# Kernel optimization log

Hardware: AMD Instinct MI355X
Metric: run time of the kernel (lower is better)

## Reference

```python
import jax, jax.numpy as jnp
import numpy as np

B, S, HID, NH, KCLIP = 2, 1500, 1024, 16, 64
HD = HID // NH  # 64


def setup_inputs() -> dict:
    key = jax.random.key(0)
    ks = jax.random.split(key, 16)
    std = 0.02
    inp = {
        "query": jax.random.normal(ks[0], (B, S, HID), jnp.float32),
        "key": jax.random.normal(ks[1], (B, S, HID), jnp.float32),
        "value": jax.random.normal(ks[2], (B, S, HID), jnp.float32),
        # per-head projection weights, stacked over heads: [NH, HID, HD]
        "Wq": jax.random.normal(ks[3], (NH, HID, HD), jnp.float32) * std,
        "bq": jax.random.normal(ks[4], (NH, HD), jnp.float32) * std,
        "Wk": jax.random.normal(ks[5], (NH, HID, HD), jnp.float32) * std,
        "bk": jax.random.normal(ks[6], (NH, HD), jnp.float32) * std,
        "Wv": jax.random.normal(ks[7], (NH, HID, HD), jnp.float32) * std,
        "bv": jax.random.normal(ks[8], (NH, HD), jnp.float32) * std,
        # Shaw relative-position embedding tables: [2k+1, HD]
        "pe_k": jax.random.normal(ks[9], (2 * KCLIP + 1, HD), jnp.float32) * std,
        "pe_v": jax.random.normal(ks[10], (2 * KCLIP + 1, HD), jnp.float32) * std,
        # output projection (torch Linear stored as x @ W + b here)
        "W_fc": jax.random.normal(ks[11], (HID, HID), jnp.float32) * std,
        "b_fc": jax.random.normal(ks[12], (HID,), jnp.float32) * std,
    }
    return inp


def _rel_bias(pe, length, k_clip):
    idx = jnp.arange(length)
    dist = jnp.clip(idx[None, :] - idx[:, None], -k_clip, k_clip) + k_clip
    return pe[dist]  # [S, S, HD]


def reference(query, key, value, Wq, bq, Wk, bk, Wv, bv, pe_k, pe_v, W_fc, b_fc):
    head_dim = Wq.shape[-1]
    seq = query.shape[1]
    k_clip = (pe_k.shape[0] - 1) // 2

    kb = _rel_bias(pe_k, seq, k_clip)  # [S, S, HD]
    vb = _rel_bias(pe_v, seq, k_clip)  # [S, S, HD]

    # batched per-head projections: [B, NH, S, HD]
    Q = jnp.einsum('bsh,nhd->bnsd', query, Wq) + bq[None, :, None, :]
    K = jnp.einsum('bsh,nhd->bnsd', key, Wk) + bk[None, :, None, :]
    V = jnp.einsum('bsh,nhd->bnsd', value, Wv) + bv[None, :, None, :]

    # content term + Shaw relative-key bias term
    scores = jnp.einsum('bnqd,bnkd->bnqk', Q, K) \
           + jnp.einsum('bnqd,qkd->bnqk', Q, kb)
    scores = scores / jnp.sqrt(jnp.asarray(head_dim, scores.dtype))

    w = jax.nn.softmax(scores, axis=-1)  # [B, NH, S, S]

    out = jnp.einsum('bnqk,bnkd->bnqd', w, V) \
        + jnp.einsum('bnqk,qkd->bnqd', w, vb)

    # concat heads (head order matches ModuleList concatenation)
    hidden = out.transpose(0, 2, 1, 3).reshape(query.shape[0], seq, -1)
    return hidden @ W_fc + b_fc
```

## Files before the change

### kernel.cpp

```cpp
#include <hip/hip_runtime.h>
#include <math.h>

#define B_     2
#define S_     1500
#define HID_   1024
#define NH_    16
#define HD_    64
#define M_     (B_*S_)
#define SP_    1536

typedef short bf16x8 __attribute__((ext_vector_type(8)));
typedef short bf16x4 __attribute__((ext_vector_type(4)));
typedef float f32x4  __attribute__((ext_vector_type(4)));

__device__ __forceinline__ float b2f(short s) {
    unsigned u = ((unsigned)(unsigned short)s) << 16;
    return __uint_as_float(u);
}
__device__ __forceinline__ short f2b(float f) {
    unsigned u = __float_as_uint(f);
    unsigned r = (u + 0x7FFFu + ((u >> 16) & 1u)) >> 16;
    return (short)r;
}
__device__ __forceinline__ void gload16(const short* src, short* lds) {
    __builtin_amdgcn_global_load_lds(
        (const __attribute__((address_space(1))) void*)src,
        (__attribute__((address_space(3))) void*)lds, 16, 0, 0);
}

__global__ __launch_bounds__(256) void cvt_act3(
    const float* __restrict__ q, const float* __restrict__ k,
    const float* __restrict__ v, short* __restrict__ oq,
    short* __restrict__ ok, short* __restrict__ ov)
{
    const float* src = blockIdx.y == 0 ? q : blockIdx.y == 1 ? k : v;
    short* dst       = blockIdx.y == 0 ? oq : blockIdx.y == 1 ? ok : ov;
    int i = blockIdx.x * 256 + threadIdx.x;
    const float4* p = (const float4*)(src + (size_t)i * 8);
    float4 a = p[0], b = p[1];
    bf16x8 o;
    o[0]=f2b(a.x); o[1]=f2b(a.y); o[2]=f2b(a.z); o[3]=f2b(a.w);
    o[4]=f2b(b.x); o[5]=f2b(b.y); o[6]=f2b(b.z); o[7]=f2b(b.w);
    *(bf16x8*)(dst + (size_t)i * 8) = o;
}

__global__ __launch_bounds__(256) void prep_w(
    const float* __restrict__ Wq, const float* __restrict__ Wk,
    const float* __restrict__ Wv, const float* __restrict__ Wfc,
    const float* __restrict__ pe_k, const float* __restrict__ pe_v,
    short* __restrict__ Wqt, short* __restrict__ Wkt, short* __restrict__ Wvt,
    short* __restrict__ Wfh, short* __restrict__ Wfl,
    short* __restrict__ pe_kb, short* __restrict__ pe_vt)
{
    int z = blockIdx.x, tid = threadIdx.x;
    if (z == 1024) {
        for (int s = tid; s < 144 * 64; s += 256) {
            int j = s >> 6, d = s & 63;
            pe_kb[s] = (j < 129) ? f2b(pe_k[j * 64 + d]) : (short)0;
        }
        for (int s = tid; s < 64 * 160; s += 256) {
            int d = s / 160, j = s - d * 160;
            pe_vt[s] = (j < 129) ? f2b(pe_v[j * 64 + d]) : (short)0;
        }
        return;
    }
    __shared__ float T[64][65];
    const float* src; short* dhi; short* dlo = nullptr;
    int C, c0, r0; float scale = 1.f;
    if (z < 768) {
        int widx = z >> 8, rem = z & 255;
        int h = rem >> 4, rt = rem & 15;
        src = (widx == 0 ? Wq : widx == 1 ? Wk : Wv) + (size_t)h * 1024 * 64;
        dhi = (widx == 0 ? Wqt : widx == 1 ? Wkt : Wvt) + (size_t)h * 64 * 1024;
        scale = (widx == 0) ? 0.125f : 1.0f;
        C = 64; c0 = 0; r0 = rt * 64;
    } else {
        int idx = z - 768;
        src = Wfc; dhi = Wfh; dlo = Wfl;
        C = 1024; c0 = (idx >> 4) * 64; r0 = (idx & 15) * 64;
    }
#pragma unroll
    for (int i = 0; i < 4; ++i) {
        int slot = tid + i * 256;
        int r = slot >> 4, cg = (slot & 15) * 4;
        float4 v = *(const float4*)(src + (size_t)(r0 + r) * C + c0 + cg);
        T[r][cg+0] = v.x*scale; T[r][cg+1] = v.y*scale;
        T[r][cg+2] = v.z*scale; T[r][cg+3] = v.w*scale;
    }
    __syncthreads();
#pragma unroll
    for (int i = 0; i < 16; ++i) {
        int slot = tid + i * 256;
        int c = slot >> 6, r = slot & 63;
        float v = T[r][c];
        short hi = f2b(v);
        size_t o = (size_t)(c0 + c) * 1024 + r0 + r;
        dhi[o] = hi;
        if (dlo) dlo[o] = f2b(v - b2f(hi));
    }
}

__device__ __forceinline__ void gemm_core(
    const short* __restrict__ Ahi, const short* __restrict__ Alo,
    const short* __restrict__ Bhi, const short* __restrict__ Blo,
    int kIters, int m0, int n0, short* As, short* Bs, f32x4 (&acc)[4][4])
{
    const int tid = threadIdx.x, w = tid >> 6, lane = tid & 63;
    const int l15 = lane & 15, lr4 = lane >> 4;
    const int wr = w >> 1, wc = w & 1;

    for (int it = 0; it < kIters; ++it) {
        int kt = it * 64;
        int seg = kt >> 10, kk0 = kt & 1023;
        const short* Aseg = (seg == 1) ? Alo : Ahi;
        const short* Bseg = (seg == 2) ? Blo : Bhi;
        __syncthreads();
#pragma unroll
        for (int c = 0; c < 4; ++c) {
            int slot = (w * 4 + c) * 64 + lane;
            int r = slot >> 3, cb = slot & 7;
            int sm = m0 + r; sm = sm < M_ ? sm : M_ - 1;
            gload16(Aseg + (size_t)sm * 1024 + kk0 + ((cb ^ (r & 7)) * 8),
                    As + (size_t)(w * 4 + c) * 512);
            gload16(Bseg + (size_t)(n0 + r) * 1024 + kk0 + ((cb ^ (r & 7)) * 8),
                    Bs + (size_t)(w * 4 + c) * 512);
        }
        __syncthreads();
#pragma unroll
        for (int kh = 0; kh < 2; ++kh) {
            bf16x8 aF[4], bF[4];
#pragma unroll
            for (int mi = 0; mi < 4; ++mi) {
                int r = wr * 64 + mi * 16 + l15;
                aF[mi] = *(const bf16x8*)(As + r * 64 + (((kh*4+lr4) ^ (r & 7)) * 8));
            }
#pragma unroll
            for (int ni = 0; ni < 4; ++ni) {
                int r = wc * 64 + ni * 16 + l15;
                bF[ni] = *(const bf16x8*)(Bs + r * 64 + (((kh*4+lr4) ^ (r & 7)) * 8));
            }
#pragma unroll
            for (int mi = 0; mi < 4; ++mi)
#pragma unroll
                for (int ni = 0; ni < 4; ++ni)
                    acc[mi][ni] = __builtin_amdgcn_mfma_f32_16x16x32_bf16(
                        aF[mi], bF[ni], acc[mi][ni], 0, 0, 0);
        }
    }
}

__global__ __launch_bounds__(256) void gemm_qkv(
    const short* __restrict__ qb, const short* __restrict__ kb,
    const short* __restrict__ vb, const short* __restrict__ Wqt,
    const short* __restrict__ Wkt, const short* __restrict__ Wvt,
    const float* __restrict__ bq, const float* __restrict__ bk,
    const float* __restrict__ bv,
    short* __restrict__ Qp, short* __restrict__ Kp, short* __restrict__ Vp)
{
    __shared__ short As[128 * 64];
    __shared__ short Bs[128 * 64];
    const int z = blockIdx.z;
    const short* A  = z == 0 ? qb : z == 1 ? kb : vb;
    const short* Bw = z == 0 ? Wqt : z == 1 ? Wkt : Wvt;
    const float* bias = z == 0 ? bq : z == 1 ? bk : bv;
    const float bscale = z == 0 ? 0.125f : 1.0f;
    short* out = z == 0 ? Qp : z == 1 ? Kp : Vp;
    const int m0 = blockIdx.x * 128, n0 = blockIdx.y * 128;

    f32x4 zf = {0.f,0.f,0.f,0.f};
    f32x4 acc[4][4];
#pragma unroll
    for (int i = 0; i < 4; ++i)
#pragma unroll
        for (int j = 0; j < 4; ++j) acc[i][j] = zf;

    gemm_core(A, A, Bw, Bw, 16, m0, n0, As, Bs, acc);

    const int tid = threadIdx.x, w = tid >> 6, lane = tid & 63;
    const int l15 = lane & 15, lr4 = lane >> 4;
    const int wr = w >> 1, wc = w & 1;
#pragma unroll
    for (int mi = 0; mi < 4; ++mi)
#pragma unroll
        for (int rr = 0; rr < 4; ++rr) {
            int m = m0 + wr * 64 + mi * 16 + lr4 * 4 + rr;
            if (m >= M_) continue;
            int b = m / S_, s = m - b * S_;
#pragma unroll
            for (int ni = 0; ni < 4; ++ni) {
                int n = n0 + wc * 64 + ni * 16 + l15;
                float v = acc[mi][ni][rr] + bias[n] * bscale;
                int h = n >> 6, d = n & 63;
                out[(((size_t)(b * NH_ + h)) * S_ + s) * HD_ + d] = f2b(v);
            }
        }
}

__global__ __launch_bounds__(256) void gemm_fc(
    const short* __restrict__ Ahi, const short* __restrict__ Alo,
    const short* __restrict__ Bhi, const short* __restrict__ Blo,
    const float* __restrict__ bias, float* __restrict__ out)
{
    __shared__ short As[128 * 64];
    __shared__ short Bs[128 * 64];
    const int m0 = blockIdx.x * 128, n0 = blockIdx.y * 128;
    f32x4 zf = {0.f,0.f,0.f,0.f};
    f32x4 acc[4][4];
#pragma unroll
    for (int i = 0; i < 4; ++i)
#pragma unroll
        for (int j = 0; j < 4; ++j) acc[i][j] = zf;

    gemm_core(Ahi, Alo, Bhi, Blo, 48, m0, n0, As, Bs, acc);

    const int tid = threadIdx.x, w = tid >> 6, lane = tid & 63;
    const int l15 = lane & 15, lr4 = lane >> 4;
    const int wr = w >> 1, wc = w & 1;
#pragma unroll
    for (int mi = 0; mi < 4; ++mi)
#pragma unroll
        for (int rr = 0; rr < 4; ++rr) {
            int m = m0 + wr * 64 + mi * 16 + lr4 * 4 + rr;
            if (m >= M_) continue;
#pragma unroll
            for (int ni = 0; ni < 4; ++ni) {
                int n = n0 + wc * 64 + ni * 16 + l15;
                out[(size_t)m * 1024 + n] = acc[mi][ni][rr] + bias[n];
            }
        }
}

__global__ __launch_bounds__(256) void vtrans(
    const short* __restrict__ Vp, short* __restrict__ Vtg)
{
    __shared__ short T[64][72];
    const int bh = blockIdx.y, s0 = blockIdx.x * 64, tid = threadIdx.x;
    const size_t kv = (size_t)bh * S_ * 64;
#pragma unroll
    for (int i = 0; i < 2; ++i) {
        int slot = tid + i * 256;
        int r = slot >> 3, cb = slot & 7;
        int ss = s0 + r; ss = ss < S_ ? ss : S_ - 1;
        bf16x8 v = *(const bf16x8*)(Vp + kv + (size_t)ss * 64 + cb * 8);
        *(bf16x8*)(&T[r][cb * 8]) = v;
    }
    __syncthreads();
#pragma unroll
    for (int i = 0; i < 2; ++i) {
        int slot = tid + i * 256;
        int d = slot >> 3, cg = slot & 7;
        bf16x8 v;
#pragma unroll
        for (int j = 0; j < 8; ++j) v[j] = T[cg * 8 + j][d];
        *(bf16x8*)(Vtg + ((size_t)bh * 64 + d) * SP_ + s0 + cg * 8) = v;
    }
}

__global__ __launch_bounds__(256) void attn_mfma(
    const short* __restrict__ Qb, const short* __restrict__ Kb,
    const short* __restrict__ Vtg, const short* __restrict__ pe_kb,
    const short* __restrict__ pe_vt,
    short* __restrict__ hid_hi, short* __restrict__ hid_lo)
{
    __shared__ short Kc[64 * 64];
    __shared__ short Vt[64 * 64];
    __shared__ short qpe[64 * 144];
    __shared__ short wsm[64 * 160];
    __shared__ short Pw[4][16 * 64];

    const int tid = threadIdx.x, w = tid >> 6, lane = tid & 63;
    const int l15 = lane & 15, lr4 = lane >> 4;
    const int bh = blockIdx.y, q0 = blockIdx.x * 64;
    const int qw = q0 + w * 16;
    const int myq = qw + l15;
    const int myrow = w * 16 + l15;
    const size_t kv  = (size_t)bh * S_ * HD_;
    const size_t vtb = (size_t)bh * 64 * SP_;
    const int swz = (l15 & 7) << 1;

    {
        short ini = f2b(-1e30f);
        bf16x8 iv;
#pragma unroll
        for (int i = 0; i < 8; ++i) iv[i] = ini;
        for (int s = tid; s < 64 * 160 / 8; s += 256)
            *(bf16x8*)(wsm + (size_t)s * 8) = iv;
    }
#pragma unroll
    for (int c = 0; c < 2; ++c) {
        int slot = (w * 2 + c) * 64 + lane;
        int r = slot >> 3, cb = slot & 7;
        int sq = q0 + r; sq = sq < S_ ? sq : S_ - 1;
        gload16(Qb + kv + (size_t)sq * 64 + ((cb ^ (r & 7)) * 8),
                Kc + (size_t)(w * 2 + c) * 512);
    }
    __syncthreads();

    bf16x8 qA[2];
    {
        int r = myrow;
        qA[0] = *(const bf16x8*)(Kc + r * 64 + ((lr4 ^ (r & 7)) * 8));
        qA[1] = *(const bf16x8*)(Kc + r * 64 + (((4 + lr4) ^ (r & 7)) * 8));
    }

    f32x4 zf = {0.f,0.f,0.f,0.f};
#pragma unroll
    for (int jt = 0; jt < 9; ++jt) {
        f32x4 a = zf;
#pragma unroll
        for (int kh = 0; kh < 2; ++kh) {
            bf16x8 pf = *(const bf16x8*)(pe_kb + (size_t)(jt * 16 + l15) * 64 + kh * 32 + lr4 * 8);
            a = __builtin_amdgcn_mfma_f32_16x16x32_bf16(pf, qA[kh], a, 0, 0, 0);
        }
        bf16x4 pk;
#pragma unroll
        for (int rr = 0; rr < 4; ++rr) pk[rr] = f2b(a[rr]);
        *(bf16x4*)(qpe + (size_t)myrow * 144 + jt * 16 + lr4 * 4) = pk;
    }
    __syncthreads();

    const float qpe0   = b2f(qpe[myrow * 144 + 0]);
    const float qpe128 = b2f(qpe[myrow * 144 + 128]);

    float m = -1e30f, s0s = 0.f, s1s = 0.f;
    f32x4 o[4];
#pragma unroll
    for (int t = 0; t < 4; ++t) o[t] = zf;

    for (int c = 0; c < 24; ++c) {
        const int kc = c * 64;
        __syncthreads();
#pragma unroll
        for (int cc = 0; cc < 2; ++cc) {
            int slot = (w * 2 + cc) * 64 + lane;
            int r = slot >> 3, cb = slot & 7;
            int sk = kc + r; sk = sk < S_ ? sk : S_ - 1;
            gload16(Kb + kv + (size_t)sk * 64 + ((cb ^ (r & 7)) * 8),
                    Kc + (size_t)(w * 2 + cc) * 512);
            gload16(Vtg + vtb + (size_t)r * SP_ + kc + ((cb ^ (r & 7)) * 8),
                    Vt + (size_t)(w * 2 + cc) * 512);
        }
        __syncthreads();

        f32x4 sa[4];
#pragma unroll
        for (int t = 0; t < 4; ++t) {
            sa[t] = zf;
#pragma unroll
            for (int kh = 0; kh < 2; ++kh) {
                int r = t * 16 + l15;
                bf16x8 kB = *(const bf16x8*)(Kc + r * 64 + (((kh*4+lr4) ^ (r & 7)) * 8));
                sa[t] = __builtin_amdgcn_mfma_f32_16x16x32_bf16(kB, qA[kh], sa[t], 0, 0, 0);
            }
        }

        const bool all_lo = (kc + 63 - qw) <= -64;
        const bool all_hi = (kc - (qw + 15)) >= 64;
        const bool mixed  = !(all_lo || all_hi);
        const float ubias = all_lo ? qpe0 : qpe128;

        float lg[4][4];
        float rm = -1e30f;
#pragma unroll
        for (int t = 0; t < 4; ++t)
#pragma unroll
            for (int rr = 0; rr < 4; ++rr) {
                int k = kc + t * 16 + lr4 * 4 + rr;
                int rel = k - myq;
                float v;
                if (mixed) {
                    int jc = rel < -64 ? 0 : (rel > 64 ? 128 : rel + 64);
                    v = sa[t][rr] + b2f(qpe[myrow * 144 + jc]);
                } else {
                    v = sa[t][rr] + ubias;
                }
                if (k >= S_) v = -1e30f;
                lg[t][rr] = v;
                rm = fmaxf(rm, v);
                if (mixed && rel > -64 && rel < 64)
                    wsm[myrow * 160 + rel + 64] = f2b(v);
            }
        rm = fmaxf(rm, __shfl_xor(rm, 16));
        rm = fmaxf(rm, __shfl_xor(rm, 32));

        if (__any(rm > m)) {
            float nm = fmaxf(m, rm);
            float fac = __expf(m - nm);
            m = nm; s0s *= fac; s1s *= fac;
            float fo[4];
#pragma unroll
            for (int rr = 0; rr < 4; ++rr) fo[rr] = __shfl(fac, lr4 * 4 + rr);
#pragma unroll
            for (int t = 0; t < 4; ++t)
#pragma unroll
                for (int rr = 0; rr < 4; ++rr) o[t][rr] *= fo[rr];
        }

        float ls0 = 0.f, ls1 = 0.f;
#pragma unroll
        for (int t = 0; t < 4; ++t) {
            bf16x4 pk;
#pragma unroll
            for (int rr = 0; rr < 4; ++rr) {
                float p = __expf(lg[t][rr] - m);
                pk[rr] = f2b(p);
                if (mixed) {
                    int rel = (kc + t * 16 + lr4 * 4 + rr) - myq;
                    if (rel <= -64) ls0 += p; else if (rel >= 64) ls1 += p;
                } else if (all_lo) ls0 += p; else ls1 += p;
            }
            *(bf16x4*)(Pw[w] + l15 * 64 + (((t * 4 + lr4) ^ swz) << 2)) = pk;
        }
        ls0 += __shfl_xor(ls0, 16); ls0 += __shfl_xor(ls0, 32);
        ls1 += __shfl_xor(ls1, 16); ls1 += __shfl_xor(ls1, 32);
        s0s += ls0; s1s += ls1;

#pragma unroll
        for (int win = 0; win < 2; ++win) {
            bf16x8 pA = *(const bf16x8*)(Pw[w] + l15 * 64 + (((win * 8 + lr4 * 2) ^ swz) << 2));
#pragma unroll
            for (int td = 0; td < 4; ++td) {
                int r = td * 16 + l15;
                bf16x8 vB = *(const bf16x8*)(Vt + r * 64 + (((win*4+lr4) ^ (r & 7)) * 8));
                o[td] = __builtin_amdgcn_mfma_f32_16x16x32_bf16(pA, vB, o[td], 0, 0, 0);
            }
        }
    }

    short* rowp = wsm + (size_t)myrow * 160;
    float midsum = 0.f;
#pragma unroll
    for (int cc = 0; cc < 5; ++cc) {
        int off = (cc * 4 + lr4) * 8;
        bf16x8 mv = *(const bf16x8*)(rowp + off);
        bf16x8 ev;
#pragma unroll
        for (int jj = 0; jj < 8; ++jj) {
            float e = __expf(b2f(mv[jj]) - m);
            ev[jj] = f2b(e);
            midsum += e;
        }
        *(bf16x8*)(rowp + off) = ev;
    }
    midsum += __shfl_xor(midsum, 16); midsum += __shfl_xor(midsum, 32);
    const float linv = 1.f / (s0s + s1s + midsum);
    if (lr4 == 0) { rowp[0] = f2b(s0s); rowp[128] = f2b(s1s); }

#pragma unroll
    for (int jh = 0; jh < 5; ++jh) {
        bf16x8 aW = *(const bf16x8*)(wsm + (size_t)myrow * 160 + jh * 32 + lr4 * 8);
#pragma unroll
        for (int td = 0; td < 4; ++td) {
            bf16x8 bW = *(const bf16x8*)(pe_vt + (size_t)(td * 16 + l15) * 160 + jh * 32 + lr4 * 8);
            o[td] = __builtin_amdgcn_mfma_f32_16x16x32_bf16(aW, bW, o[td], 0, 0, 0);
        }
    }

    {
        float fo[4];
#pragma unroll
        for (int rr = 0; rr < 4; ++rr) fo[rr] = __shfl(linv, lr4 * 4 + rr);
#pragma unroll
        for (int td = 0; td < 4; ++td)
#pragma unroll
            for (int rr = 0; rr < 4; ++rr) o[td][rr] *= fo[rr];
    }

#pragma unroll
    for (int td = 0; td < 4; ++td)
#pragma unroll
        for (int rr = 0; rr < 4; ++rr) {
            int qrow = lr4 * 4 + rr;
            int d = td * 16 + l15;
            int inner = (((d >> 2) ^ ((qrow & 7) << 1)) << 2) + (d & 3);
            float v = o[td][rr];
            short hi = f2b(v);
            Pw[w][qrow * 64 + inner] = hi;
            wsm[(w * 16 + qrow) * 160 + inner] = f2b(v - b2f(hi));
        }
    {
        int b = bh >> 4, h = bh & 15;
        int qrow = lane >> 2;
        int q = q0 + w * 16 + qrow;
#pragma unroll
        for (int i = 0; i < 2; ++i) {
            int cb = (lane & 3) * 2 + i;
            int qws = (cb * 2) ^ ((qrow & 7) << 1);
            bf16x8 hv = *(const bf16x8*)(Pw[w] + qrow * 64 + qws * 4);
            bf16x8 lv = *(const bf16x8*)(wsm + (w * 16 + qrow) * 160 + qws * 4);
            if (q < S_) {
                size_t oo = ((size_t)(b * S_ + q)) * 1024 + h * 64 + cb * 8;
                *(bf16x8*)(hid_hi + oo) = hv;
                *(bf16x8*)(hid_lo + oo) = lv;
            }
        }
    }
}

extern "C" void kernel_launch(void* const* d_in, const int* in_sizes, int n_in,
                              void* d_out, int out_size, void* d_ws, size_t ws_size,
                              hipStream_t stream)
{
    const float* query = (const float*)d_in[0];
    const float* key   = (const float*)d_in[1];
    const float* value = (const float*)d_in[2];
    const float* Wq    = (const float*)d_in[3];
    const float* bq    = (const float*)d_in[4];
    const float* Wk    = (const float*)d_in[5];
    const float* bk    = (const float*)d_in[6];
    const float* Wv    = (const float*)d_in[7];
    const float* bv    = (const float*)d_in[8];
    const float* pe_k  = (const float*)d_in[9];
    const float* pe_v  = (const float*)d_in[10];
    const float* W_fc  = (const float*)d_in[11];
    const float* b_fc  = (const float*)d_in[12];

    char* W = (char*)d_ws;
    short* qb   = (short*)(W + 0);
    short* kb   = (short*)(W + 6291456);
    short* vb   = (short*)(W + 12582912);
    short* Vtg  = vb;
    short* Wqt  = (short*)(W + 18874368);
    short* Wkt  = (short*)(W + 20971520);
    short* Wvt  = (short*)(W + 23068672);
    short* Wfh  = (short*)(W + 25165824);
    short* Wfl  = (short*)(W + 27262976);
    short* Qp   = (short*)(W + 29360128);
    short* Kp   = (short*)(W + 35651584);
    short* Vp   = (short*)(W + 41943040);
    short* pekb = (short*)(W + 48234496);
    short* pevt = (short*)(W + 48252928);
    short* hidh = qb;
    short* hidl = kb;

    cvt_act3<<<dim3(1500, 3), 256, 0, stream>>>(query, key, value, qb, kb, vb);
    prep_w<<<1025, 256, 0, stream>>>(Wq, Wk, Wv, W_fc, pe_k, pe_v,
                                     Wqt, Wkt, Wvt, Wfh, Wfl, pekb, pevt);
    gemm_qkv<<<dim3(24, 8, 3), 256, 0, stream>>>(qb, kb, vb, Wqt, Wkt, Wvt,
                                                 bq, bk, bv, Qp, Kp, Vp);
    vtrans<<<dim3(24, 32), 256, 0, stream>>>(Vp, Vtg);
    attn_mfma<<<dim3(24, 32), 256, 0, stream>>>(Qp, Kp, Vtg, pekb, pevt, hidh, hidl);
    gemm_fc<<<dim3(24, 8), 256, 0, stream>>>(hidh, hidl, Wfh, Wfl, b_fc, (float*)d_out);
}
```

Before: 284.3 us.

## Use exp2 softmax with lazy rescale, XCD-aware block remap and MFMA priority

The Q weight and bias scale now includes log2(e), so the attention kernel can use exp2f for softmax instead of __expf. The online-softmax rescale is skipped unless the new row max exceeds the running max by more than 8 in the log2 domain. The grid is flattened and remapped so that consecutive blocks on the same XCD work on the same batch-head, which should improve L2 reuse of K and V. The code also adds s_setprio around the MFMA sections, moves the loop barrier to the end of each iteration, and gives each wave its own slice of the wsm init. The lazy rescale lets unnormalised probabilities grow up to 256 before rescaling, which may cost some bf16 precision.

After: 289.2 us. Within noise of the previous version (+1.7%).

```diff
diff --git a/kernel.cpp b/kernel.cpp
--- a/kernel.cpp
+++ b/kernel.cpp
@@ -8,6 +8,7 @@
 #define HD_    64
 #define M_     (B_*S_)
 #define SP_    1536
+#define LOG2E  1.4426950408889634f
 
 typedef short bf16x8 __attribute__((ext_vector_type(8)));
 typedef short bf16x4 __attribute__((ext_vector_type(4)));
@@ -72,7 +73,7 @@
         int h = rem >> 4, rt = rem & 15;
         src = (widx == 0 ? Wq : widx == 1 ? Wk : Wv) + (size_t)h * 1024 * 64;
         dhi = (widx == 0 ? Wqt : widx == 1 ? Wkt : Wvt) + (size_t)h * 64 * 1024;
-        scale = (widx == 0) ? 0.125f : 1.0f;
+        scale = (widx == 0) ? 0.125f * LOG2E : 1.0f;
         C = 64; c0 = 0; r0 = rt * 64;
     } else {
         int idx = z - 768;
@@ -163,7 +164,7 @@
     const short* A  = z == 0 ? qb : z == 1 ? kb : vb;
     const short* Bw = z == 0 ? Wqt : z == 1 ? Wkt : Wvt;
     const float* bias = z == 0 ? bq : z == 1 ? bk : bv;
-    const float bscale = z == 0 ? 0.125f : 1.0f;
+    const float bscale = z == 0 ? 0.125f * LOG2E : 1.0f;
     short* out = z == 0 ? Qp : z == 1 ? Kp : Vp;
     const int m0 = blockIdx.x * 128, n0 = blockIdx.y * 128;
 
@@ -262,15 +263,17 @@
     const short* __restrict__ pe_vt,
     short* __restrict__ hid_hi, short* __restrict__ hid_lo)
 {
-    __shared__ short Kc[64 * 64];
-    __shared__ short Vt[64 * 64];
+    __shared__ short Kc[4096];
+    __shared__ short Vt[4096];
     __shared__ short qpe[64 * 144];
     __shared__ short wsm[64 * 160];
-    __shared__ short Pw[4][16 * 64];
+    __shared__ short Pw[4][1024];
 
     const int tid = threadIdx.x, w = tid >> 6, lane = tid & 63;
     const int l15 = lane & 15, lr4 = lane >> 4;
-    const int bh = blockIdx.y, q0 = blockIdx.x * 64;
+    const int lg = (blockIdx.x & 7) * 96 + (blockIdx.x >> 3);
+    const int bh = lg / 24, bx = lg - bh * 24;
+    const int q0 = bx * 64;
     const int qw = q0 + w * 16;
     const int myq = qw + l15;
     const int myrow = w * 16 + l15;
@@ -283,16 +286,18 @@
         bf16x8 iv;
 #pragma unroll
         for (int i = 0; i < 8; ++i) iv[i] = ini;
-        for (int s = tid; s < 64 * 160 / 8; s += 256)
-            *(bf16x8*)(wsm + (size_t)s * 8) = iv;
-    }
-#pragma unroll
-    for (int c = 0; c < 2; ++c) {
-        int slot = (w * 2 + c) * 64 + lane;
+        short* base = wsm + w * 16 * 160;
+#pragma unroll
+        for (int i = 0; i < 5; ++i)
+            *(bf16x8*)(base + (size_t)(i * 64 + lane) * 8) = iv;
+    }
+#pragma unroll
+    for (int cc = 0; cc < 2; ++cc) {
+        int slot = (w * 2 + cc) * 64 + lane;
         int r = slot >> 3, cb = slot & 7;
         int sq = q0 + r; sq = sq < S_ ? sq : S_ - 1;
         gload16(Qb + kv + (size_t)sq * 64 + ((cb ^ (r & 7)) * 8),
-                Kc + (size_t)(w * 2 + c) * 512);
+                Kc + (size_t)(w * 2 + cc) * 512);
     }
     __syncthreads();
 
@@ -317,10 +322,9 @@
         for (int rr = 0; rr < 4; ++rr) pk[rr] = f2b(a[rr]);
         *(bf16x4*)(qpe + (size_t)myrow * 144 + jt * 16 + lr4 * 4) = pk;
     }
-    __syncthreads();
-
     const float qpe0   = b2f(qpe[myrow * 144 + 0]);
     const float qpe128 = b2f(qpe[myrow * 144 + 128]);
+    __syncthreads();
 
     float m = -1e30f, s0s = 0.f, s1s = 0.f;
     f32x4 o[4];
@@ -329,7 +333,6 @@
 
     for (int c = 0; c < 24; ++c) {
         const int kc = c * 64;
-        __syncthreads();
 #pragma unroll
         for (int cc = 0; cc < 2; ++cc) {
             int slot = (w * 2 + cc) * 64 + lane;
@@ -342,6 +345,7 @@
         }
         __syncthreads();
 
+        __builtin_amdgcn_s_setprio(1);
         f32x4 sa[4];
 #pragma unroll
         for (int t = 0; t < 4; ++t) {
@@ -353,13 +357,14 @@
                 sa[t] = __builtin_amdgcn_mfma_f32_16x16x32_bf16(kB, qA[kh], sa[t], 0, 0, 0);
             }
         }
+        __builtin_amdgcn_s_setprio(0);
 
         const bool all_lo = (kc + 63 - qw) <= -64;
         const bool all_hi = (kc - (qw + 15)) >= 64;
         const bool mixed  = !(all_lo || all_hi);
         const float ubias = all_lo ? qpe0 : qpe128;
 
-        float lg[4][4];
+        float lg2[4][4];
         float rm = -1e30f;
 #pragma unroll
         for (int t = 0; t < 4; ++t)
@@ -375,7 +380,7 @@
                     v = sa[t][rr] + ubias;
                 }
                 if (k >= S_) v = -1e30f;
-                lg[t][rr] = v;
+                lg2[t][rr] = v;
                 rm = fmaxf(rm, v);
                 if (mixed && rel > -64 && rel < 64)
                     wsm[myrow * 160 + rel + 64] = f2b(v);
@@ -383,9 +388,9 @@
         rm = fmaxf(rm, __shfl_xor(rm, 16));
         rm = fmaxf(rm, __shfl_xor(rm, 32));
 
-        if (__any(rm > m)) {
+        if (!__all(rm <= m + 8.f)) {
             float nm = fmaxf(m, rm);
-            float fac = __expf(m - nm);
+            float fac = exp2f(m - nm);
             m = nm; s0s *= fac; s1s *= fac;
             float fo[4];
 #pragma unroll
@@ -402,12 +407,12 @@
             bf16x4 pk;
 #pragma unroll
             for (int rr = 0; rr < 4; ++rr) {
-                float p = __expf(lg[t][rr] - m);
-                pk[rr] = f2b(p);
+                float p2 = exp2f(lg2[t][rr] - m);
+                pk[rr] = f2b(p2);
                 if (mixed) {
                     int rel = (kc + t * 16 + lr4 * 4 + rr) - myq;
-                    if (rel <= -64) ls0 += p; else if (rel >= 64) ls1 += p;
-                } else if (all_lo) ls0 += p; else ls1 += p;
+                    if (rel <= -64) ls0 += p2; else if (rel >= 64) ls1 += p2;
+                } else if (all_lo) ls0 += p2; else ls1 += p2;
             }
             *(bf16x4*)(Pw[w] + l15 * 64 + (((t * 4 + lr4) ^ swz) << 2)) = pk;
         }
@@ -415,6 +420,7 @@
         ls1 += __shfl_xor(ls1, 16); ls1 += __shfl_xor(ls1, 32);
         s0s += ls0; s1s += ls1;
 
+        __builtin_amdgcn_s_setprio(1);
 #pragma unroll
         for (int win = 0; win < 2; ++win) {
             bf16x8 pA = *(const bf16x8*)(Pw[w] + l15 * 64 + (((win * 8 + lr4 * 2) ^ swz) << 2));
@@ -425,6 +431,9 @@
                 o[td] = __builtin_amdgcn_mfma_f32_16x16x32_bf16(pA, vB, o[td], 0, 0, 0);
             }
         }
+        __builtin_amdgcn_s_setprio(0);
+
+        __syncthreads();
     }
 
     short* rowp = wsm + (size_t)myrow * 160;
@@ -436,7 +445,7 @@
         bf16x8 ev;
 #pragma unroll
         for (int jj = 0; jj < 8; ++jj) {
-            float e = __expf(b2f(mv[jj]) - m);
+            float e = exp2f(b2f(mv[jj]) - m);
             ev[jj] = f2b(e);
             midsum += e;
         }
@@ -539,6 +548,6 @@
     gemm_qkv<<<dim3(24, 8, 3), 256, 0, stream>>>(qb, kb, vb, Wqt, Wkt, Wvt,
                                                  bq, bk, bv, Qp, Kp, Vp);
     vtrans<<<dim3(24, 32), 256, 0, stream>>>(Vp, Vtg);
-    attn_mfma<<<dim3(24, 32), 256, 0, stream>>>(Qp, Kp, Vtg, pekb, pevt, hidh, hidl);
+    attn_mfma<<<768, 256, 0, stream>>>(Qp, Kp, Vtg, pekb, pevt, hidh, hidl);
     gemm_fc<<<dim3(24, 8), 256, 0, stream>>>(hidh, hidl, Wfh, Wfl, b_fc, (float*)d_out);
 }
```
